# Kernel tuning notes

Measured on AMD Instinct MI355X. Metric: run time of the kernel, lower is better.

The kernel has to match this reference:

```python
import jax, jax.numpy as jnp
import numpy as np

NUM_GRAPHS = 128
EPS = 1e-5  # torch BatchNorm1d default eps


def setup_inputs() -> dict:
    key = jax.random.key(0)
    ks = jax.random.split(key, 24)
    N, E, NHE = 50000, 800000, 50000
    NODE_RAW, HEDGE_RAW, H, HH, HOUT = 92, 40, 128, 128, 256
    s = 0.05
    inp = {
        "x": jax.random.normal(ks[0], (N, NODE_RAW), jnp.float32),
        "hedge_attrs": jax.random.normal(ks[1], (NHE, HEDGE_RAW), jnp.float32),
        "inter_relations_index": jax.random.randint(ks[2], (3, E), 0, N, jnp.int64),
        "batch": jax.random.randint(ks[3], (N,), 0, NUM_GRAPHS, jnp.int64),
        "num_nodes": N,
        # embed: Linear(92, h_dim)
        "embed_w": jax.random.normal(ks[4], (NODE_RAW, H), jnp.float32) * s,
        "embed_b": jax.random.normal(ks[5], (H,), jnp.float32) * s,
        # bembed: Linear(hedge_dim, hidden_hedge_dim)
        "bembed_w": jax.random.normal(ks[6], (HEDGE_RAW, HH), jnp.float32) * s,
        "bembed_b": jax.random.normal(ks[7], (HH,), jnp.float32) * s,
        # conv.lin_full_presplit: Linear(2H+HH, 2H)
        "lin_w": jax.random.normal(ks[8], (2 * H + HH, 2 * H), jnp.float32) * s,
        "lin_b": jax.random.normal(ks[9], (2 * H,), jnp.float32) * s,
        "bn1_g": jnp.ones((2 * H,), jnp.float32),
        "bn1_b": jnp.zeros((2 * H,), jnp.float32),
        "bn2_g": jnp.ones((H,), jnp.float32),
        "bn2_b": jnp.zeros((H,), jnp.float32),
        # learnable temperature of SoftmaxAggregation (init 1.0)
        "aggr_t": jnp.ones((), jnp.float32),
        "l1_w": jax.random.normal(ks[10], (H, HOUT), jnp.float32) * s,
        "l1_b": jax.random.normal(ks[11], (HOUT,), jnp.float32) * s,
        "out_w": jax.random.normal(ks[12], (HOUT, 1), jnp.float32) * s,
        "out_b": jax.random.normal(ks[13], (1,), jnp.float32) * s,
    }
    return inp


def _batchnorm(z, g, b):
    mu = z.mean(axis=0)
    var = z.var(axis=0)  # biased, matching torch training-mode normalization
    return (z - mu) * jax.lax.rsqrt(var + EPS) * g + b


def reference(x, hedge_attrs, inter_relations_index, batch, num_nodes,
              embed_w, embed_b, bembed_w, bembed_b, lin_w, lin_b,
              bn1_g, bn1_b, bn2_g, bn2_b, aggr_t, l1_w, l1_b, out_w, out_b):
    idx0 = inter_relations_index[0]
    idx1 = inter_relations_index[1]
    connect_feats = hedge_attrs @ bembed_w + bembed_b          # [NHE, HH]
    h = x @ embed_w + embed_b                                   # [N, H]

    # --- CHGInterConv ---
    origin = h[idx0]                                            # [E, H]
    connect = connect_feats[idx1]                               # [E, HH]
    remote = h[idx0]                                            # faithful to source (uses idx0)
    z = jnp.concatenate([origin, connect, remote], axis=1)      # [E, 2H+HH]
    z = z @ lin_w + lin_b                                       # [E, 2H]
    z = _batchnorm(z, bn1_g, bn1_b)
    z_f, z_c = jnp.split(z, 2, axis=-1)
    msg = jax.nn.sigmoid(z_f) * jax.nn.softplus(z_c)            # [E, H]

    # learned SoftmaxAggregation: per-node, per-channel segment softmax of t*msg
    alpha = msg * aggr_t
    m = jax.ops.segment_max(alpha, idx0, num_segments=num_nodes)
    m = jnp.where(jnp.isfinite(m), m, 0.0)                      # empty segments
    e = jnp.exp(alpha - m[idx0])
    denom = jax.ops.segment_sum(e, idx0, num_segments=num_nodes)
    w = e / (denom[idx0] + 1e-16)
    out = jax.ops.segment_sum(msg * w, idx0, num_segments=num_nodes)  # [N, H]

    out = _batchnorm(out, bn2_g, bn2_b)
    h = jax.nn.softplus(out + h)                                # residual + softplus

    # --- global mean pool over graphs ---
    counts = jax.ops.segment_sum(jnp.ones((num_nodes,), h.dtype), batch,
                                 num_segments=NUM_GRAPHS)
    pooled = jax.ops.segment_sum(h, batch, num_segments=NUM_GRAPHS)
    pooled = pooled / jnp.maximum(counts, 1.0)[:, None]         # [G, H]

    g = jax.nn.softplus(pooled @ l1_w + l1_b)                   # [G, HOUT]
    return g @ out_w + out_b                                    # [G, 1]
```

## Files before the change

kernel.cpp:

```cpp
#include <hip/hip_runtime.h>
#include <hip/hip_bf16.h>


#define EPS_BN 1e-5f
#define LOG2E 1.4426950408889634f
#define LN2   0.6931471805599453f

#define BIN_SH 8
#define BIN_CHUNK 4096

typedef __attribute__((ext_vector_type(8))) short bf16x8;
typedef __attribute__((ext_vector_type(4))) float f32x4;
typedef __attribute__((ext_vector_type(2))) float f32x2;

__device__ __forceinline__ float fexp2(float x) {
#if __has_builtin(__builtin_amdgcn_exp2f)
    return __builtin_amdgcn_exp2f(x);
#else
    return __expf(x * LN2);
#endif
}
__device__ __forceinline__ float flog2(float x) {
#if __has_builtin(__builtin_amdgcn_logf)
    return __builtin_amdgcn_logf(x);
#else
    return __logf(x) * LOG2E;
#endif
}
__device__ __forceinline__ float softplus_fast(float x) {
    return LN2 * flog2(1.f + fexp2(x * LOG2E));
}

__device__ __forceinline__ f32x2 pk_fma2(f32x2 a, f32x2 b, f32x2 c) {
#if __has_builtin(__builtin_elementwise_fma)
    return __builtin_elementwise_fma(a, b, c);
#else
    return (f32x2){fmaf(a.x, b.x, c.x), fmaf(a.y, b.y, c.y)};
#endif
}

__device__ __forceinline__ unsigned short f2bf(float f) {
    unsigned u = __float_as_uint(f);
    unsigned r = (u + 0x7fffu + ((u >> 16) & 1u)) >> 16;
    return (unsigned short)r;
}
__device__ __forceinline__ float bflo(unsigned u) { return __uint_as_float(u << 16); }
__device__ __forceinline__ float bfhi(unsigned u) { return __uint_as_float(u & 0xffff0000u); }
__device__ __forceinline__ float bfu16(unsigned short v) { return __uint_as_float(((unsigned)v) << 16); }
__device__ __forceinline__ unsigned pack2bf(float x, float y) {
    return (unsigned)f2bf(x) | ((unsigned)f2bf(y) << 16);
}

#if __has_builtin(__builtin_amdgcn_cvt_pk_f32_fp8) && __has_builtin(__builtin_amdgcn_cvt_pk_fp8_f32)
#define HW_FP8 1
#else
#define HW_FP8 0
#endif

__device__ __forceinline__ unsigned char f2fp8(float f) {
#if HW_FP8
    int r = __builtin_amdgcn_cvt_pk_fp8_f32(f, f, 0, false);
    return (unsigned char)(r & 0xff);
#else
    unsigned u = __float_as_uint(f);
    unsigned s = (u >> 24) & 0x80u;
    float af = fabsf(f);
    if (!(af >= 0.015625f)) {
        int m = (int)rintf(af * 512.f);
        if (m > 7) m = 7;
        return (unsigned char)(s | (unsigned)m);
    }
    if (af > 448.f) return (unsigned char)(s | 0x7e);
    unsigned au = __float_as_uint(af);
    unsigned r = au + 0x7ffffu + ((au >> 20) & 1u);
    int e8 = (int)(r >> 23) - 120;
    unsigned m = (r >> 20) & 7u;
    if (e8 > 15 || (e8 == 15 && m == 7)) return (unsigned char)(s | 0x7e);
    return (unsigned char)(s | ((unsigned)e8 << 3) | m);
#endif
}

__device__ __forceinline__ void fp8pair(unsigned p, f32x2& lo, f32x2& hi) {
#if HW_FP8
    lo = __builtin_amdgcn_cvt_pk_f32_fp8((int)p, false);
    hi = __builtin_amdgcn_cvt_pk_f32_fp8((int)p, true);
#else
    auto dec = [](unsigned byte) -> float {
        unsigned s = (byte & 0x80u) << 24;
        unsigned em = byte & 0x7fu;
        float nrm = __uint_as_float(s | ((em << 20) + 0x3C000000u));
        float sub = __uint_as_float(s | 0x3F800000u) * (float)em * 0.001953125f;
        return (em >= 8) ? nrm : sub;
    };
    lo = (f32x2){dec(p & 0xff), dec((p >> 8) & 0xff)};
    hi = (f32x2){dec((p >> 16) & 0xff), dec(p >> 24)};
#endif
}

__device__ __forceinline__ int perm256(int j) {
    return (j < 128) ? ((j >> 1) * 4 + (j & 1)) : (((j - 128) >> 1) * 4 + 2 + (j & 1));
}

__global__ __launch_bounds__(256) void k_prepw(const float* __restrict__ ew, const float* __restrict__ bw,
                                               const float* __restrict__ lw,
                                               unsigned short* __restrict__ embB, unsigned short* __restrict__ bembB,
                                               unsigned short* __restrict__ waB, unsigned short* __restrict__ wcB) {
    int i = blockIdx.x * 256 + threadIdx.x;
    if (i >= 81920) return;
    unsigned short* dst;
    int f, NKC, CT, mode;
    if (i < 12288)      { dst = embB;  f = i;         NKC = 3; CT = 2; mode = 0; }
    else if (i < 20480) { dst = bembB; f = i - 12288; NKC = 2; CT = 2; mode = 1; }
    else if (i < 53248) { dst = waB;   f = i - 20480; NKC = 4; CT = 4; mode = 2; }
    else                { dst = wcB;   f = i - 53248; NKC = 4; CT = 4; mode = 3; }
    int j = f & 7, l = (f >> 3) & 63;
    int r2 = f >> 9;
    int c = r2 % CT;
    int r3 = r2 / CT;
    int kc = r3 % NKC, w = r3 / NKC;
    int k = kc * 32 + ((l >> 4) & 3) * 8 + j;
    int n = (w * CT + c) * 16 + (l & 15);
    float v;
    if (mode == 0)      v = (k < 92) ? ew[k * 128 + n] : 0.f;
    else if (mode == 1) v = (k < 40) ? bw[k * 128 + n] : 0.f;
    else if (mode == 2) v = lw[k * 256 + n] + lw[(k + 256) * 256 + n];
    else                v = lw[(k + 128) * 256 + n];
    dst[f] = f2bf(v);
}

template<int KIN, int NKC1, int OMODE2>
__global__ __launch_bounds__(256) void mfma_fused(
    const float* __restrict__ in, const unsigned short* __restrict__ B1, const float* __restrict__ bias1,
    const unsigned short* __restrict__ B2, const float* __restrict__ bias2,
    unsigned short* __restrict__ hout, void* __restrict__ out2, int M,
    const int* __restrict__ aux_idx, int* __restrict__ aux_hist, int aux_cnt)
{
    const int r0 = blockIdx.x * 32;
    const int t = threadIdx.x;
    const int w = t >> 6;
    const int l = t & 63;
    const int m = l & 15, q = l >> 4;

    if (aux_idx) {
        const int T = gridDim.x * 256;
        for (int i = blockIdx.x * 256 + t; i < aux_cnt; i += T)
            atomicAdd(&aux_hist[aux_idx[i]], 1);
    }

    __shared__ __align__(16) unsigned short als[32 * NKC1 * 32];
    __shared__ __align__(16) unsigned short hls[32 * 136];

    const int KP = NKC1 * 32;
    for (int i = t; i < 32 * KP; i += 256) {
        int r = i / KP, k = i - r * KP;
        int gr = r0 + r;
        float v = (gr < M && k < KIN) ? in[(size_t)gr * KIN + k] : 0.f;
        int idx = (((r >> 4) * NKC1 + (k >> 5)) * 64 + ((k >> 3) & 3) * 16 + (r & 15)) * 8 + (k & 7);
        als[idx] = f2bf(v);
    }
    bf16x8 b1[NKC1][2];
    const bf16x8* B1f = (const bf16x8*)B1;
#pragma unroll
    for (int kc = 0; kc < NKC1; kc++)
#pragma unroll
        for (int c = 0; c < 2; c++)
            b1[kc][c] = B1f[((w * NKC1 + kc) * 2 + c) * 64 + l];
    __syncthreads();

    f32x4 acc1[2][2];
#pragma unroll
    for (int c = 0; c < 2; c++) { acc1[c][0] = (f32x4){0.f,0.f,0.f,0.f}; acc1[c][1] = (f32x4){0.f,0.f,0.f,0.f}; }
    const bf16x8* af = (const bf16x8*)als;
#pragma unroll
    for (int kc = 0; kc < NKC1; kc++) {
        bf16x8 a0 = af[kc * 64 + l];
        bf16x8 a1 = af[(NKC1 + kc) * 64 + l];
#pragma unroll
        for (int c = 0; c < 2; c++) {
            acc1[c][0] = __builtin_amdgcn_mfma_f32_16x16x32_bf16(a0, b1[kc][c], acc1[c][0], 0, 0, 0);
            acc1[c][1] = __builtin_amdgcn_mfma_f32_16x16x32_bf16(a1, b1[kc][c], acc1[c][1], 0, 0, 0);
        }
    }
#pragma unroll
    for (int c = 0; c < 2; c++) {
        int n1 = (w * 2 + c) * 16 + m;
        float bv = bias1[n1];
#pragma unroll
        for (int hh = 0; hh < 2; hh++) {
#pragma unroll
            for (int r = 0; r < 4; r++) {
                int row = hh * 16 + q * 4 + r;
                float val = acc1[c][hh][r] + bv;
                unsigned short bf = f2bf(val);
                hls[row * 136 + n1] = bf;
                if (OMODE2 == 1 && r0 + row < M) hout[(size_t)(r0 + row) * 128 + n1] = bf;
            }
        }
    }
    __syncthreads();

    bf16x8 b2[4][4];
    const bf16x8* B2f = (const bf16x8*)B2;
#pragma unroll
    for (int kc = 0; kc < 4; kc++)
#pragma unroll
        for (int c = 0; c < 4; c++)
            b2[kc][c] = B2f[((w * 4 + kc) * 4 + c) * 64 + l];

    f32x4 acc2[4][2];
#pragma unroll
    for (int c = 0; c < 4; c++) { acc2[c][0] = (f32x4){0.f,0.f,0.f,0.f}; acc2[c][1] = (f32x4){0.f,0.f,0.f,0.f}; }
#pragma unroll
    for (int kc = 0; kc < 4; kc++) {
        bf16x8 a0 = *(const bf16x8*)(hls + m * 136 + kc * 32 + q * 8);
        bf16x8 a1 = *(const bf16x8*)(hls + (m + 16) * 136 + kc * 32 + q * 8);
#pragma unroll
        for (int c = 0; c < 4; c++) {
            acc2[c][0] = __builtin_amdgcn_mfma_f32_16x16x32_bf16(a0, b2[kc][c], acc2[c][0], 0, 0, 0);
            acc2[c][1] = __builtin_amdgcn_mfma_f32_16x16x32_bf16(a1, b2[kc][c], acc2[c][1], 0, 0, 0);
        }
    }
#pragma unroll
    for (int c = 0; c < 4; c++) {
        int n = (w * 4 + c) * 16 + m;
        float bv = bias2 ? bias2[n] : 0.f;
        int pj = perm256(n);
#pragma unroll
        for (int hh = 0; hh < 2; hh++) {
#pragma unroll
            for (int r = 0; r < 4; r++) {
                int row = r0 + hh * 16 + q * 4 + r;
                if (row < M) {
                    float val = acc2[c][hh][r] + bv;
                    if (OMODE2 == 1) ((unsigned short*)out2)[(size_t)row * 256 + pj] = f2bf(val);
                    else             ((unsigned char*)out2)[(size_t)row * 256 + pj] = f2fp8(val);
                }
            }
        }
    }
}

__global__ __launch_bounds__(256) void k_scanA(const int* __restrict__ hist, int* __restrict__ rloc,
                                               int* __restrict__ bsum, int N) {
    __shared__ int s[256];
    const int t = threadIdx.x;
    const int n0 = blockIdx.x << 8;
    const int nn = min(N - n0, 256);
    int v = (t < nn) ? hist[n0 + t] : 0;
    s[t] = v;
    __syncthreads();
#pragma unroll
    for (int ofs = 1; ofs < 256; ofs <<= 1) {
        int u = (t >= ofs) ? s[t - ofs] : 0;
        __syncthreads();
        s[t] += u;
        __syncthreads();
    }
    if (t < nn) rloc[n0 + t] = s[t] - v;
    if (t == 255) bsum[blockIdx.x] = s[255];
}

__global__ __launch_bounds__(256) void k_scanB(const int* __restrict__ bsum, int* __restrict__ boff,
                                               const int* __restrict__ gcount, int* __restrict__ gptr, int NB) {
    __shared__ int s[256];
    const int t = threadIdx.x;
    int v = (t < NB) ? bsum[t] : 0;
    s[t] = v;
    __syncthreads();
#pragma unroll
    for (int ofs = 1; ofs < 256; ofs <<= 1) {
        int u = (t >= ofs) ? s[t - ofs] : 0;
        __syncthreads();
        s[t] += u;
        __syncthreads();
    }
    if (t < NB) boff[t] = s[t] - v;
    if (t == NB - 1) boff[NB] = s[t];
    __syncthreads();
    int gv = (t < 128) ? gcount[t] : 0;
    s[t] = gv;
    __syncthreads();
#pragma unroll
    for (int ofs = 1; ofs < 128; ofs <<= 1) {
        int u = (t >= ofs && t < 128) ? s[t - ofs] : 0;
        __syncthreads();
        if (t < 128) s[t] += u;
        __syncthreads();
    }
    if (t < 128) gptr[t + 1] = s[t];
    if (t == 0) gptr[0] = 0;
}

__global__ __launch_bounds__(256) void k_binA(
    const int* __restrict__ idx0, const int* __restrict__ idx1,
    const int* __restrict__ boff, const int* __restrict__ rloc,
    int* __restrict__ rowptr, int* __restrict__ bfill,
    int* __restrict__ staging,
    const int* __restrict__ batch, const int* __restrict__ gptr,
    int* __restrict__ gfill, int* __restrict__ gnodes,
    int E, int N, int NB, int EB, int GB)
{
    const int t = threadIdx.x;
    const int bid = blockIdx.x;
    if (bid >= EB + GB) {
        int i = ((bid - EB - GB) << 8) + t;
        if (i < N) rowptr[i] = boff[i >> BIN_SH] + rloc[i];
        if (bid == EB + GB && t == 0) rowptr[N] = boff[NB];
        return;
    }
    if (bid >= EB) {
        int i = (bid - EB) * 256 + t;
        if (i < N) {
            int g = batch[i];
            int pos = gptr[g] + atomicAdd(&gfill[g], 1);
            gnodes[pos] = i;
        }
        return;
    }
    __shared__ int svals[BIN_CHUNK];
    __shared__ unsigned char sbk[BIN_CHUNK];
    __shared__ int lhist[256], lbase[256];
    const int e0 = bid * BIN_CHUNK;
    const int cnt = min(E - e0, BIN_CHUNK);
    for (int b = t; b < NB; b += 256) lhist[b] = 0;
    __syncthreads();
    for (int i = t; i < cnt; i += 256) {
        int n = idx0[e0 + i];
        int m = idx1[e0 + i];
        int bk = n >> BIN_SH;
        sbk[i] = (unsigned char)bk;
        svals[i] = (m << BIN_SH) | (n & ((1 << BIN_SH) - 1));
        atomicAdd(&lhist[bk], 1);
    }
    __syncthreads();
    for (int b = t; b < NB; b += 256) {
        int h = lhist[b];
        int base = h ? atomicAdd(&bfill[b], h) : 0;
        lbase[b] = boff[b] + base;
        lhist[b] = 0;
    }
    __syncthreads();
    for (int i = t; i < cnt; i += 256) {
        int bk = sbk[i];
        int r = atomicAdd(&lhist[bk], 1);
        staging[lbase[bk] + r] = svals[i];
    }
}

__global__ __launch_bounds__(256) void k_build2(
    const int* __restrict__ rowptr, const int* __restrict__ staging,
    int* __restrict__ sidx1, int2* __restrict__ slots,
    const uint2* __restrict__ A16, const int* __restrict__ hist0,
    float* __restrict__ gsum, float* __restrict__ gsq,
    int E, int N, int per_slot, int nslots, int NB, int SL_BLOCKS)
{
    __shared__ float4 lsm4[256], lsq4[256];
    __shared__ int rp[257];
    __shared__ int lcnt[256];
    const int t = threadIdx.x;
    const int bid = blockIdx.x;

    if (bid < NB) {
        const int n0 = bid << BIN_SH;
        const int nn = min(N - n0, 256);
        for (int j = t; j <= nn; j += 256) rp[j] = rowptr[n0 + j];
        lcnt[t] = 0;
        __syncthreads();
        const int s0 = rp[0], s1 = rp[nn];
        for (int i = s0 + t; i < s1; i += 256) {
            int v = staging[i];
            int nl = v & 255;
            int r = atomicAdd(&lcnt[nl], 1);
            sidx1[rp[nl] + r] = v & 0xffffff00;
        }
        return;
    }
    if (bid < NB + SL_BLOCKS) {
        int s = (bid - NB) * 256 + t;
        if (s > nslots) return;
        long base = (long)s * per_slot;
        if (base >= E) { slots[s] = (int2){N, N - 1}; return; }
        int e0 = (int)base;
        int lo = 0, hi = N;
        while (lo + 1 < hi) { int mid = (lo + hi) >> 1; if (rowptr[mid] <= e0) lo = mid; else hi = mid; }
        int nS = lo;
        int nA = 0;
        if (e0 > 0) {
            lo = 0; hi = N;
            while (lo + 1 < hi) { int mid = (lo + hi) >> 1; if (rowptr[mid] < e0) lo = mid; else hi = mid; }
            nA = hi;
        }
        slots[s] = (int2){nA, nS};
        return;
    }
    const int s = t >> 6, l = t & 63;
    const int rb = bid - NB - SL_BLOCKS;
    const int w0 = rb * 4 + s;
    const int nw = (gridDim.x - NB - SL_BLOCKS) * 4;
    f32x2 smF = {0.f,0.f}, smC = {0.f,0.f}, sqF = {0.f,0.f}, sqC = {0.f,0.f};
    for (int n = w0; n < N; n += nw) {
        float dg = (float)hist0[n];
        uint2 a8 = A16[(size_t)n * 64 + l];
        f32x2 aF = {bflo(a8.x), bfhi(a8.x)};
        f32x2 aC = {bflo(a8.y), bfhi(a8.y)};
        f32x2 dF = aF * dg;
        f32x2 dC = aC * dg;
        smF += dF; smC += dC;
        sqF = pk_fma2(dF, aF, sqF);
        sqC = pk_fma2(dC, aC, sqC);
    }
    lsm4[t] = (float4){smF.x, smF.y, smC.x, smC.y};
    lsq4[t] = (float4){sqF.x, sqF.y, sqC.x, sqC.y};
    __syncthreads();
    const float* fm = (const float*)lsm4;
    const float* fq = (const float*)lsq4;
    float vs = fm[t] + fm[256 + t] + fm[512 + t] + fm[768 + t];
    float vq = fq[t] + fq[256 + t] + fq[512 + t] + fq[768 + t];
    atomicAdd(&gsum[t], vs);
    atomicAdd(&gsq[t], vq);
}

__global__ __launch_bounds__(256) void k_stats(const uint2* __restrict__ A16, const unsigned char* __restrict__ Cp8b,
                                               const int* __restrict__ rowptr, const int* __restrict__ sidx1,
                                               const int2* __restrict__ slots,
                                               float* __restrict__ gsum, float* __restrict__ gsq,
                                               int E, int N, int per_slot) {
    __shared__ float4 lsm4[256], lsq4[256];
    const int t = threadIdx.x;
    const int l = t & 63;
    const int wid = __builtin_amdgcn_readfirstlane(t >> 6);
    const int slot = blockIdx.x * 4 + wid;
    const unsigned lo4 = (unsigned)(l << 2);
    const long base = (long)slot * per_slot;
    const int e0 = (int)min((long)E, base);
    const int e1 = (int)min((long)E, base + per_slot);
    f32x2 smF = {0.f,0.f}, smC = {0.f,0.f};
    f32x2 sqF = {0.f,0.f}, sqC = {0.f,0.f};
    f32x2 csrF = {0.f,0.f}, csrC = {0.f,0.f};
    f32x2 aF2 = {0.f,0.f}, aC2 = {0.f,0.f};
    int cur_n = 0, bound = 0;

    auto flush = [&]() {
        smF += csrF; smC += csrC;
        sqF = pk_fma2(aF2, csrF, sqF);
        sqC = pk_fma2(aC2, csrC, sqC);
        csrF = (f32x2){0.f,0.f}; csrC = (f32x2){0.f,0.f};
    };
    auto loadA = [&](int n) {
        uint2 a8 = A16[(size_t)n * 64 + l];
        aF2 = (f32x2){bflo(a8.x) * 2.f, bfhi(a8.x) * 2.f};
        aC2 = (f32x2){bflo(a8.y) * 2.f, bfhi(a8.y) * 2.f};
    };

    if (e0 < e1) {
        cur_n = __builtin_amdgcn_readfirstlane(slots[slot].y);
        bound = __builtin_amdgcn_readfirstlane(rowptr[cur_n + 1]);
        loadA(cur_n);
    }

    auto proc = [&](int e, unsigned p) {
        if (e >= bound) {
            flush();
            do { cur_n++; bound = __builtin_amdgcn_readfirstlane(rowptr[cur_n + 1]); } while (bound <= e);
            loadA(cur_n);
        }
        f32x2 vf, vc;
        fp8pair(p, vf, vc);
        csrF += vf; csrC += vc;
        sqF = pk_fma2(vf, vf, sqF);
        sqC = pk_fma2(vc, vc, sqC);
    };

    const int nfull = (e1 - e0) & ~7;
    if (nfull > 0) {
        int eg = e0;
        unsigned cur[8];
        {
            int4 m0 = *(const int4*)(sidx1 + eg);
            int4 m1 = *(const int4*)(sidx1 + eg + 4);
            cur[0] = *(const unsigned*)(Cp8b + ((unsigned)m0.x + lo4));
            cur[1] = *(const unsigned*)(Cp8b + ((unsigned)m0.y + lo4));
            cur[2] = *(const unsigned*)(Cp8b + ((unsigned)m0.z + lo4));
            cur[3] = *(const unsigned*)(Cp8b + ((unsigned)m0.w + lo4));
            cur[4] = *(const unsigned*)(Cp8b + ((unsigned)m1.x + lo4));
            cur[5] = *(const unsigned*)(Cp8b + ((unsigned)m1.y + lo4));
            cur[6] = *(const unsigned*)(Cp8b + ((unsigned)m1.z + lo4));
            cur[7] = *(const unsigned*)(Cp8b + ((unsigned)m1.w + lo4));
        }
        for (;;) {
            const int en = eg + 8;
            const bool more = en < e0 + nfull;
            unsigned nxt[8];
            if (more) {
                int4 t0 = *(const int4*)(sidx1 + en);
                int4 t1 = *(const int4*)(sidx1 + en + 4);
                nxt[0] = *(const unsigned*)(Cp8b + ((unsigned)t0.x + lo4));
                nxt[1] = *(const unsigned*)(Cp8b + ((unsigned)t0.y + lo4));
                nxt[2] = *(const unsigned*)(Cp8b + ((unsigned)t0.z + lo4));
                nxt[3] = *(const unsigned*)(Cp8b + ((unsigned)t0.w + lo4));
                nxt[4] = *(const unsigned*)(Cp8b + ((unsigned)t1.x + lo4));
                nxt[5] = *(const unsigned*)(Cp8b + ((unsigned)t1.y + lo4));
                nxt[6] = *(const unsigned*)(Cp8b + ((unsigned)t1.z + lo4));
                nxt[7] = *(const unsigned*)(Cp8b + ((unsigned)t1.w + lo4));
            }
            proc(eg, cur[0]);     proc(eg + 1, cur[1]);
            proc(eg + 2, cur[2]); proc(eg + 3, cur[3]);
            proc(eg + 4, cur[4]); proc(eg + 5, cur[5]);
            proc(eg + 6, cur[6]); proc(eg + 7, cur[7]);
            if (!more) break;
#pragma unroll
            for (int i = 0; i < 8; i++) cur[i] = nxt[i];
            eg = en;
        }
    }
    for (int e = e0 + nfull; e < e1; e++)
        proc(e, *(const unsigned*)(Cp8b + ((unsigned)sidx1[e] + lo4)));
    flush();

    lsm4[t] = (float4){smF.x, smF.y, smC.x, smC.y};
    lsq4[t] = (float4){sqF.x, sqF.y, sqC.x, sqC.y};
    __syncthreads();
    const float* fm = (const float*)lsm4;
    const float* fq = (const float*)lsq4;
    float vs = fm[t] + fm[256 + t] + fm[512 + t] + fm[768 + t];
    float vq = fq[t] + fq[256 + t] + fq[512 + t] + fq[768 + t];
    atomicAdd(&gsum[t], vs);
    atomicAdd(&gsq[t], vq);
}

__global__ __launch_bounds__(256) void k_aggr(const uint2* __restrict__ A16, const unsigned char* __restrict__ Cp8b,
                                              const int* __restrict__ rowptr, const int* __restrict__ sidx1,
                                              const float* __restrict__ bn1_sum, const float* __restrict__ bn1_sq,
                                              const float* __restrict__ g1, const float* __restrict__ b1,
                                              const float* __restrict__ tptr, unsigned* __restrict__ out,
                                              float invE, int N) {
    const int t = threadIdx.x;
    const int l = t & 63;
    const int wid = __builtin_amdgcn_readfirstlane(t >> 6);
    const int n = blockIdx.x * 4 + wid;
    if (n >= N) return;

    const int e0 = __builtin_amdgcn_readfirstlane(rowptr[n]);
    const int e1 = __builtin_amdgcn_readfirstlane(rowptr[n + 1]);

    const float tt = tptr[0];
    const float4 sum4 = ((const float4*)bn1_sum)[l];
    const float4 sq4  = ((const float4*)bn1_sq)[l];
    const float2 gf = ((const float2*)g1)[l];
    const float2 gc = ((const float2*)(g1 + 128))[l];
    const float2 bf2 = ((const float2*)b1)[l];
    const float2 bc2 = ((const float2*)(b1 + 128))[l];
    auto mkss = [&](float sum, float sq, float gg, float bb, float& sc, float& sh) {
        float mu = sum * invE;
        float var = sq * invE - mu * mu;
        sc = gg * rsqrtf(var + EPS_BN);
        sh = fmaf(-mu, sc, bb);
    };
    float scx, shx, scy, shy, scz, shz, scw, shw;
    mkss(sum4.x, sq4.x, gf.x, bf2.x, scx, shx);
    mkss(sum4.y, sq4.y, gf.y, bf2.y, scy, shy);
    mkss(sum4.z, sq4.z, gc.x, bc2.x, scz, shz);
    mkss(sum4.w, sq4.w, gc.y, bc2.y, scw, shw);
    const f32x2 sF  = {-scx * LOG2E, -scy * LOG2E};
    const f32x2 sC  = { scz * LOG2E,  scw * LOG2E};

    uint2 a8 = A16[(size_t)n * 64 + l];
    f32x2 aF = {bflo(a8.x), bfhi(a8.x)}, aC = {bflo(a8.y), bfhi(a8.y)};
    const f32x2 bF = pk_fma2(aF, sF, (f32x2){-shx * LOG2E, -shy * LOG2E});
    const f32x2 bC = pk_fma2(aC, sC, (f32x2){ shz * LOG2E,  shw * LOG2E});

    if (e0 >= e1) { out[(size_t)n * 64 + l] = 0u; return; }

    const unsigned lo4 = (unsigned)(l << 2);
    f32x2 den = {0.f,0.f}, num = {0.f,0.f};

    auto G = [&](int e) -> unsigned {
        return *(const unsigned*)(Cp8b + ((unsigned)sidx1[e] + lo4));
    };
    auto procg = [&](unsigned p) {
        f32x2 vf, vc;
        fp8pair(p, vf, vc);
        f32x2 argf = pk_fma2(vf, sF, bF);
        f32x2 argc = pk_fma2(vc, sC, bC);
        f32x2 ef = {fexp2(argf.x), fexp2(argf.y)};
        f32x2 uu = {fexp2(argc.x), fexp2(argc.y)};
        f32x2 d1 = ef + 1.f;
        f32x2 u1 = uu + 1.f;
        f32x2 sig = {__builtin_amdgcn_rcpf(d1.x), __builtin_amdgcn_rcpf(d1.y)};
        f32x2 lg = {flog2(u1.x), flog2(u1.y)};
        f32x2 M = sig * lg;
        f32x2 tM = M * tt;
        f32x2 w = {fexp2(tM.x), fexp2(tM.y)};
        den += w;
        num = pk_fma2(M, w, num);
    };

    const int cnt = e1 - e0;
    unsigned cur[8];
#pragma unroll
    for (int i = 0; i < 8; i++)
        if (i < cnt) cur[i] = G(e0 + i);

    int e = e0;
    while (e + 8 < e1) {
        unsigned nxt[8];
#pragma unroll
        for (int i = 0; i < 8; i++)
            if (e + 8 + i < e1) nxt[i] = G(e + 8 + i);
#pragma unroll
        for (int i = 0; i < 8; i++) procg(cur[i]);
#pragma unroll
        for (int i = 0; i < 8; i++) cur[i] = nxt[i];
        e += 8;
    }
    const int rem = e1 - e;
#pragma unroll
    for (int i = 0; i < 8; i++)
        if (i < rem) procg(cur[i]);

    float ox = LN2 * num.x * __builtin_amdgcn_rcpf(den.x);
    float oy = LN2 * num.y * __builtin_amdgcn_rcpf(den.y);
    out[(size_t)n * 64 + l] = pack2bf(ox, oy);
}

__global__ __launch_bounds__(256) void k_bn2stats(const unsigned* __restrict__ outw, float* __restrict__ sum,
                                                  float* __restrict__ sq, int N) {
    __shared__ float4 ls[256];
    const int t = threadIdx.x;
    const int w = t & 63;
    const int rg = t >> 6;
    f32x2 sm = {0.f,0.f}, s2 = {0.f,0.f};
    for (int n = blockIdx.x * 4 + rg; n < N; n += gridDim.x * 4) {
        unsigned v = outw[(size_t)n * 64 + w];
        f32x2 x = {bflo(v), bfhi(v)};
        sm += x;
        s2 = pk_fma2(x, x, s2);
    }
    ls[t] = (float4){sm.x, sm.y, s2.x, s2.y};
    __syncthreads();
    if (t < 64) {
        float4 a = ls[t], b = ls[t + 64], c = ls[t + 128], d = ls[t + 192];
        atomicAdd(&sum[2 * w],     a.x + b.x + c.x + d.x);
        atomicAdd(&sum[2 * w + 1], a.y + b.y + c.y + d.y);
        atomicAdd(&sq[2 * w],      a.z + b.z + c.z + d.z);
        atomicAdd(&sq[2 * w + 1],  a.w + b.w + c.w + d.w);
    }
}

template<int SPLIT>
__global__ __launch_bounds__(128) void k_h2pool(const unsigned short* __restrict__ out,
                                                const unsigned short* __restrict__ h,
                                                const int* __restrict__ gptr, const int* __restrict__ gnodes,
                                                const float* __restrict__ bn2_sum, const float* __restrict__ bn2_sq,
                                                const float* __restrict__ g2, const float* __restrict__ b2,
                                                float* __restrict__ pooled, float invN) {
    const int g = blockIdx.x & 127;
    const int sp = blockIdx.x >> 7;
    const int c = threadIdx.x;
    float mu = bn2_sum[c] * invN;
    float var = bn2_sq[c] * invN - mu * mu;
    float sc = g2[c] * rsqrtf(var + EPS_BN);
    float sh = fmaf(-mu, sc, b2[c]);
    const int i0 = gptr[g], i1 = gptr[g + 1];
    float acc = 0.f;
    for (int i = i0 + sp; i < i1; i += SPLIT) {
        int n = gnodes[i];
        float v = fmaf(bfu16(out[(size_t)n * 128 + c]), sc, sh) + bfu16(h[(size_t)n * 128 + c]);
        acc += softplus_fast(v);
    }
    if (acc != 0.f) atomicAdd(&pooled[g * 128 + c], acc);
}

__global__ __launch_bounds__(256) void k_head(const float* __restrict__ pooled, const int* __restrict__ gcount,
                                              const float* __restrict__ l1w, const float* __restrict__ l1b,
                                              const float* __restrict__ outw, const float* __restrict__ outb,
                                              float* __restrict__ dout) {
    __shared__ float p[128];
    __shared__ float red[256];
    const int g = blockIdx.x;
    const int j = threadIdx.x;
    if (j < 128) {
        float cnt = (float)max(gcount[g], 1);
        p[j] = pooled[g * 128 + j] / cnt;
    }
    __syncthreads();
    float acc = l1b[j];
    for (int k = 0; k < 128; k++) acc = fmaf(p[k], l1w[k * 256 + j], acc);
    red[j] = softplus_fast(acc) * outw[j];
    __syncthreads();
    for (int s = 128; s > 0; s >>= 1) {
        if (j < s) red[j] += red[j + s];
        __syncthreads();
    }
    if (j == 0) dout[g] = red[0] + outb[0];
}

extern "C" void kernel_launch(void* const* d_in, const int* in_sizes, int n_in,
                              void* d_out, int out_size, void* d_ws, size_t ws_size,
                              hipStream_t stream) {
    const float* x        = (const float*)d_in[0];
    const float* hedge    = (const float*)d_in[1];
    const int*   iri      = (const int*)d_in[2];
    const int*   batch    = (const int*)d_in[3];
    const float* embed_w  = (const float*)d_in[5];
    const float* embed_b  = (const float*)d_in[6];
    const float* bembed_w = (const float*)d_in[7];
    const float* bembed_b = (const float*)d_in[8];
    const float* lin_w    = (const float*)d_in[9];
    const float* lin_b    = (const float*)d_in[10];
    const float* bn1_g    = (const float*)d_in[11];
    const float* bn1_b    = (const float*)d_in[12];
    const float* bn2_g    = (const float*)d_in[13];
    const float* bn2_b    = (const float*)d_in[14];
    const float* aggr_t   = (const float*)d_in[15];
    const float* l1_w     = (const float*)d_in[16];
    const float* l1_b     = (const float*)d_in[17];
    const float* out_w    = (const float*)d_in[18];
    const float* out_b    = (const float*)d_in[19];

    const int N   = in_sizes[0] / 92;
    const int NHE = in_sizes[1] / 40;
    const int E   = in_sizes[2] / 3;
    const int* idx0 = iri;
    const int* idx1 = iri + E;

    float* ws = (float*)d_ws;
    size_t off = 0;
    auto alloc = [&](size_t elems) -> float* {
        float* p = ws + off;
        off += (elems + 63) & ~(size_t)63;
        return p;
    };
    unsigned short* h16 = (unsigned short*)alloc((size_t)N * 64);
    uint2* A16    = (uint2*)alloc((size_t)N * 128);
    unsigned* Cp8 = (unsigned*)alloc((size_t)NHE * 64);
    unsigned short* embB  = (unsigned short*)alloc(6144);
    unsigned short* bembB = (unsigned short*)alloc(4096);
    unsigned short* waB   = (unsigned short*)alloc(16384);
    unsigned short* wcB   = (unsigned short*)alloc(16384);
    int*   rowptr = (int*)alloc((size_t)N + 1);
    int*   rloc   = (int*)alloc((size_t)N);
    int*   bsum   = (int*)alloc(256);
    int*   boff   = (int*)alloc(260);
    int*   sidx1  = (int*)alloc((size_t)E + 8);
    int*   staging = (int*)alloc((size_t)E + 8);
    int*   gptr   = (int*)alloc(129);
    int*   gnodes = (int*)alloc((size_t)N);
    unsigned* outbuf = (unsigned*)alloc((size_t)N * 64);
    int2*  slots  = (int2*)alloc(2 * 8200);
    float* zbase  = ws + off;
    int*   hist   = (int*)alloc((size_t)N);
    int*   bfill  = (int*)alloc(256);
    int*   gfill  = (int*)alloc(128);
    float* bn1_sum = alloc(256);
    float* bn1_sq  = alloc(256);
    float* bn2_sum = alloc(128);
    float* bn2_sq  = alloc(128);
    float* pooled  = alloc(128 * 128);
    int*   gcount  = (int*)alloc(128);
    size_t zbytes = (size_t)((ws + off) - zbase) * sizeof(float);
    (void)ws_size;

    hipMemsetAsync(zbase, 0, zbytes, stream);

    k_prepw<<<320, 256, 0, stream>>>(embed_w, bembed_w, lin_w, embB, bembB, waB, wcB);
    const int mtN   = (N + 31) / 32;
    const int mtNHE = (NHE + 31) / 32;
    mfma_fused<92, 3, 1><<<mtN, 256, 0, stream>>>(x, embB, embed_b, waB, lin_b, h16, A16, N,
                                                  idx0, hist, E);
    mfma_fused<40, 2, 2><<<mtNHE, 256, 0, stream>>>(hedge, bembB, bembed_b, wcB, nullptr, nullptr, Cp8, NHE,
                                                    batch, gcount, N);

    const int NB = (N + 255) >> BIN_SH;
    k_scanA<<<NB, 256, 0, stream>>>(hist, rloc, bsum, N);
    k_scanB<<<1, 256, 0, stream>>>(bsum, boff, gcount, gptr, NB);

    const int EB = (E + BIN_CHUNK - 1) / BIN_CHUNK;
    const int GB = (N + 255) / 256;
    k_binA<<<EB + GB + NB, 256, 0, stream>>>(idx0, idx1, boff, rloc, rowptr, bfill, staging,
                                             batch, gptr, gfill, gnodes, E, N, NB, EB, GB);

    const int EDGE_BLOCKS = 2048;
    const int NSLOTS = EDGE_BLOCKS * 4;
    int per_slot = ((E + NSLOTS - 1) / NSLOTS + 7) & ~7;
    int nslots_used = (E + per_slot - 1) / per_slot;

    const int SL_BLOCKS = (nslots_used + 1 + 255) / 256;
    const int RS_BLOCKS = 256;
    k_build2<<<NB + SL_BLOCKS + RS_BLOCKS, 256, 0, stream>>>(
        rowptr, staging, sidx1, slots, A16, hist, bn1_sum, bn1_sq,
        E, N, per_slot, nslots_used, NB, SL_BLOCKS);

    k_stats<<<EDGE_BLOCKS, 256, 0, stream>>>(A16, (const unsigned char*)Cp8, rowptr, sidx1, slots,
                                             bn1_sum, bn1_sq, E, N, per_slot);

    k_aggr<<<(N + 3) / 4, 256, 0, stream>>>(A16, (const unsigned char*)Cp8, rowptr, sidx1,
                                            bn1_sum, bn1_sq, bn1_g, bn1_b, aggr_t, outbuf,
                                            1.0f / (float)E, N);

    k_bn2stats<<<256, 256, 0, stream>>>((const unsigned*)outbuf, bn2_sum, bn2_sq, N);
    k_h2pool<16><<<128 * 16, 128, 0, stream>>>((const unsigned short*)outbuf, h16, gptr, gnodes,
                                               bn2_sum, bn2_sq, bn2_g, bn2_b, pooled, 1.0f / (float)N);

    k_head<<<128, 256, 0, stream>>>(pooled, gcount, l1_w, l1_b, out_w, out_b, (float*)d_out);
}
```

Before: 476.2 us.

## Fold per-node BN1 stat pass into edge stats and move slot search into binning

The separate per-node pass in k_build2, which read A16 weighted by degree to build the BN1 sum and sum-of-squares terms, is removed. k_stats now counts edges per node run and adds the node-side contributions (k*a and a*(2*csr + k*a)) when it flushes. The slot binary search moves into k_binA and computes rowptr from boff+rloc, leaving k_binB to do only the CSR scatter. This drops a full read of A16 over all nodes and one kernel's worth of work, at the cost of slightly more arithmetic per flush and a more expensive rowptr lookup inside the binary search.

```diff
diff --git a/kernel.cpp b/kernel.cpp
--- a/kernel.cpp
+++ b/kernel.cpp
@@ -298,10 +298,30 @@
     int* __restrict__ staging,
     const int* __restrict__ batch, const int* __restrict__ gptr,
     int* __restrict__ gfill, int* __restrict__ gnodes,
-    int E, int N, int NB, int EB, int GB)
+    int2* __restrict__ slots,
+    int E, int N, int NB, int EB, int GB, int per_slot, int nslots)
 {
     const int t = threadIdx.x;
     const int bid = blockIdx.x;
+    if (bid >= EB + GB + NB) {
+        int s = (bid - EB - GB - NB) * 256 + t;
+        if (s > nslots) return;
+        long base = (long)s * per_slot;
+        if (base >= E) { slots[s] = (int2){N, N - 1}; return; }
+        int e0 = (int)base;
+        auto rp = [&](int n) { return boff[n >> BIN_SH] + rloc[n]; };
+        int lo = 0, hi = N;
+        while (lo + 1 < hi) { int mid = (lo + hi) >> 1; if (rp(mid) <= e0) lo = mid; else hi = mid; }
+        int nS = lo;
+        int nA = 0;
+        if (e0 > 0) {
+            lo = 0; hi = N;
+            while (lo + 1 < hi) { int mid = (lo + hi) >> 1; if (rp(mid) < e0) lo = mid; else hi = mid; }
+            nA = hi;
+        }
+        slots[s] = (int2){nA, nS};
+        return;
+    }
     if (bid >= EB + GB) {
         int i = ((bid - EB - GB) << 8) + t;
         if (i < N) rowptr[i] = boff[i >> BIN_SH] + rloc[i];
@@ -347,77 +367,25 @@
     }
 }
 
-__global__ __launch_bounds__(256) void k_build2(
+__global__ __launch_bounds__(256) void k_binB(
     const int* __restrict__ rowptr, const int* __restrict__ staging,
-    int* __restrict__ sidx1, int2* __restrict__ slots,
-    const uint2* __restrict__ A16, const int* __restrict__ hist0,
-    float* __restrict__ gsum, float* __restrict__ gsq,
-    int E, int N, int per_slot, int nslots, int NB, int SL_BLOCKS)
+    int* __restrict__ sidx1, int N)
 {
-    __shared__ float4 lsm4[256], lsq4[256];
     __shared__ int rp[257];
     __shared__ int lcnt[256];
     const int t = threadIdx.x;
-    const int bid = blockIdx.x;
-
-    if (bid < NB) {
-        const int n0 = bid << BIN_SH;
-        const int nn = min(N - n0, 256);
-        for (int j = t; j <= nn; j += 256) rp[j] = rowptr[n0 + j];
-        lcnt[t] = 0;
-        __syncthreads();
-        const int s0 = rp[0], s1 = rp[nn];
-        for (int i = s0 + t; i < s1; i += 256) {
-            int v = staging[i];
-            int nl = v & 255;
-            int r = atomicAdd(&lcnt[nl], 1);
-            sidx1[rp[nl] + r] = v & 0xffffff00;
-        }
-        return;
-    }
-    if (bid < NB + SL_BLOCKS) {
-        int s = (bid - NB) * 256 + t;
-        if (s > nslots) return;
-        long base = (long)s * per_slot;
-        if (base >= E) { slots[s] = (int2){N, N - 1}; return; }
-        int e0 = (int)base;
-        int lo = 0, hi = N;
-        while (lo + 1 < hi) { int mid = (lo + hi) >> 1; if (rowptr[mid] <= e0) lo = mid; else hi = mid; }
-        int nS = lo;
-        int nA = 0;
-        if (e0 > 0) {
-            lo = 0; hi = N;
-            while (lo + 1 < hi) { int mid = (lo + hi) >> 1; if (rowptr[mid] < e0) lo = mid; else hi = mid; }
-            nA = hi;
-        }
-        slots[s] = (int2){nA, nS};
-        return;
-    }
-    const int s = t >> 6, l = t & 63;
-    const int rb = bid - NB - SL_BLOCKS;
-    const int w0 = rb * 4 + s;
-    const int nw = (gridDim.x - NB - SL_BLOCKS) * 4;
-    f32x2 smF = {0.f,0.f}, smC = {0.f,0.f}, sqF = {0.f,0.f}, sqC = {0.f,0.f};
-    for (int n = w0; n < N; n += nw) {
-        float dg = (float)hist0[n];
-        uint2 a8 = A16[(size_t)n * 64 + l];
-        f32x2 aF = {bflo(a8.x), bfhi(a8.x)};
-        f32x2 aC = {bflo(a8.y), bfhi(a8.y)};
-        f32x2 dF = aF * dg;
-        f32x2 dC = aC * dg;
-        smF += dF; smC += dC;
-        sqF = pk_fma2(dF, aF, sqF);
-        sqC = pk_fma2(dC, aC, sqC);
-    }
-    lsm4[t] = (float4){smF.x, smF.y, smC.x, smC.y};
-    lsq4[t] = (float4){sqF.x, sqF.y, sqC.x, sqC.y};
-    __syncthreads();
-    const float* fm = (const float*)lsm4;
-    const float* fq = (const float*)lsq4;
-    float vs = fm[t] + fm[256 + t] + fm[512 + t] + fm[768 + t];
-    float vq = fq[t] + fq[256 + t] + fq[512 + t] + fq[768 + t];
-    atomicAdd(&gsum[t], vs);
-    atomicAdd(&gsq[t], vq);
+    const int n0 = blockIdx.x << BIN_SH;
+    const int nn = min(N - n0, 256);
+    for (int j = t; j <= nn; j += 256) rp[j] = rowptr[n0 + j];
+    lcnt[t] = 0;
+    __syncthreads();
+    const int s0 = rp[0], s1 = rp[nn];
+    for (int i = s0 + t; i < s1; i += 256) {
+        int v = staging[i];
+        int nl = v & 255;
+        int r = atomicAdd(&lcnt[nl], 1);
+        sidx1[rp[nl] + r] = v & 0xffffff00;
+    }
 }
 
 __global__ __launch_bounds__(256) void k_stats(const uint2* __restrict__ A16, const unsigned char* __restrict__ Cp8b,
@@ -437,19 +405,28 @@
     f32x2 smF = {0.f,0.f}, smC = {0.f,0.f};
     f32x2 sqF = {0.f,0.f}, sqC = {0.f,0.f};
     f32x2 csrF = {0.f,0.f}, csrC = {0.f,0.f};
-    f32x2 aF2 = {0.f,0.f}, aC2 = {0.f,0.f};
-    int cur_n = 0, bound = 0;
+    f32x2 aF = {0.f,0.f}, aC = {0.f,0.f};
+    int cur_n = 0, bound = 0, runk = 0;
 
     auto flush = [&]() {
-        smF += csrF; smC += csrC;
-        sqF = pk_fma2(aF2, csrF, sqF);
-        sqC = pk_fma2(aC2, csrC, sqC);
+        if (runk) {
+            float fk = (float)runk;
+            f32x2 fk2 = {fk, fk};
+            smF += csrF; smC += csrC;
+            smF = pk_fma2(fk2, aF, smF);
+            smC = pk_fma2(fk2, aC, smC);
+            f32x2 tF = pk_fma2(fk2, aF, csrF + csrF);
+            f32x2 tC = pk_fma2(fk2, aC, csrC + csrC);
+            sqF = pk_fma2(aF, tF, sqF);
+            sqC = pk_fma2(aC, tC, sqC);
+        }
         csrF = (f32x2){0.f,0.f}; csrC = (f32x2){0.f,0.f};
+        runk = 0;
     };
     auto loadA = [&](int n) {
         uint2 a8 = A16[(size_t)n * 64 + l];
-        aF2 = (f32x2){bflo(a8.x) * 2.f, bfhi(a8.x) * 2.f};
-        aC2 = (f32x2){bflo(a8.y) * 2.f, bfhi(a8.y) * 2.f};
+        aF = (f32x2){bflo(a8.x), bfhi(a8.x)};
+        aC = (f32x2){bflo(a8.y), bfhi(a8.y)};
     };
 
     if (e0 < e1) {
@@ -469,6 +446,7 @@
         csrF += vf; csrC += vc;
         sqF = pk_fma2(vf, vf, sqF);
         sqC = pk_fma2(vc, vc, sqC);
+        runk++;
     };
 
     const int nfull = (e1 - e0) & ~7;
@@ -775,21 +753,19 @@
     k_scanA<<<NB, 256, 0, stream>>>(hist, rloc, bsum, N);
     k_scanB<<<1, 256, 0, stream>>>(bsum, boff, gcount, gptr, NB);
 
-    const int EB = (E + BIN_CHUNK - 1) / BIN_CHUNK;
-    const int GB = (N + 255) / 256;
-    k_binA<<<EB + GB + NB, 256, 0, stream>>>(idx0, idx1, boff, rloc, rowptr, bfill, staging,
-                                             batch, gptr, gfill, gnodes, E, N, NB, EB, GB);
-
     const int EDGE_BLOCKS = 2048;
     const int NSLOTS = EDGE_BLOCKS * 4;
     int per_slot = ((E + NSLOTS - 1) / NSLOTS + 7) & ~7;
     int nslots_used = (E + per_slot - 1) / per_slot;
 
+    const int EB = (E + BIN_CHUNK - 1) / BIN_CHUNK;
+    const int GB = (N + 255) / 256;
     const int SL_BLOCKS = (nslots_used + 1 + 255) / 256;
-    const int RS_BLOCKS = 256;
-    k_build2<<<NB + SL_BLOCKS + RS_BLOCKS, 256, 0, stream>>>(
-        rowptr, staging, sidx1, slots, A16, hist, bn1_sum, bn1_sq,
-        E, N, per_slot, nslots_used, NB, SL_BLOCKS);
+    k_binA<<<EB + GB + NB + SL_BLOCKS, 256, 0, stream>>>(
+        idx0, idx1, boff, rloc, rowptr, bfill, staging,
+        batch, gptr, gfill, gnodes, slots, E, N, NB, EB, GB, per_slot, nslots_used);
+
+    k_binB<<<NB, 256, 0, stream>>>(rowptr, staging, sidx1, N);
 
     k_stats<<<EDGE_BLOCKS, 256, 0, stream>>>(A16, (const unsigned char*)Cp8, rowptr, sidx1, slots,
                                              bn1_sum, bn1_sq, E, N, per_slot);
```

New measurement: 466.9 us. About the same (-2.0%).
